# Kernel tuning notes

Hardware: AMD Instinct MI355X
Metric: run time of the kernel (lower is better)

The kernel has to match this reference:

```python
import jax, jax.numpy as jnp
import numpy as np

# Standard SMPL kinematic tree (24 joints), parent of joint i
PARENTS = np.array([-1, 0, 0, 0, 1, 2, 3, 4, 5, 6, 7, 8, 9, 9, 9,
                    12, 13, 14, 16, 17, 18, 19, 20, 21])
N_JOINTS = 24
EPS = 1e-8  # stands in for the tiny gaussian eps the torch code adds


def rodrigues(r):
    """Axis-angle (N,3) -> rotation matrices (N,3,3)."""
    theta = jnp.linalg.norm(r, axis=1, keepdims=True) + EPS        # (N,1)
    r_hat = r / theta                                              # (N,3)
    cos = jnp.cos(theta)[..., None]                                # (N,1,1)
    sin = jnp.sin(theta)[..., None]
    z = jnp.zeros_like(r_hat[:, 0])
    # skew-symmetric cross-product matrix of r_hat
    m = jnp.stack([z, -r_hat[:, 2], r_hat[:, 1],
                   r_hat[:, 2], z, -r_hat[:, 0],
                   -r_hat[:, 1], r_hat[:, 0], z], axis=1).reshape(-1, 3, 3)
    outer = r_hat[:, :, None] * r_hat[:, None, :]                  # (N,3,3)
    eye = jnp.eye(3, dtype=r.dtype)
    return cos * eye + (1.0 - cos) * outer + sin * m


def setup_inputs() -> dict:
    key = jax.random.key(0)
    k0, k1, k2, k3, k4 = jax.random.split(key, 5)
    B, V, J = 512, 6890, N_JOINTS
    return {
        "T_hat": jax.random.normal(k0, (V, 3), dtype=jnp.float32),
        "J_hat": jax.random.normal(k1, (J, 3), dtype=jnp.float32),
        "weights": jax.random.uniform(k2, (V, J), dtype=jnp.float32),
        "pose": jax.random.normal(k3, (B, J * 3), dtype=jnp.float32),
        "trans": jax.random.normal(k4, (B, 3), dtype=jnp.float32),
    }


def reference(T_hat, J_hat, weights, pose, trans):
    B = pose.shape[0]
    dt = pose.dtype
    # per-joint rotation matrices: (B,24,3,3)
    R = rodrigues(pose.reshape(-1, 3)).reshape(B, N_JOINTS, 3, 3)

    # relative joint offsets along the tree (24,3)
    rel_J = jnp.concatenate([J_hat[:1], J_hat[1:] - J_hat[PARENTS[1:]]], axis=0)

    # local SE(3) transforms (B,24,4,4)
    top = jnp.concatenate(
        [R, jnp.broadcast_to(rel_J[None, :, :, None], (B, N_JOINTS, 3, 1))],
        axis=-1)                                                   # (B,24,3,4)
    bottom = jnp.broadcast_to(
        jnp.array([0.0, 0.0, 0.0, 1.0], dtype=dt), (B, N_JOINTS, 1, 4))
    G_local = jnp.concatenate([top, bottom], axis=2)               # (B,24,4,4)

    # forward kinematics along the fixed 24-joint tree (small fixed loop)
    results = [G_local[:, 0]]
    for i in range(1, N_JOINTS):
        results.append(jnp.matmul(results[PARENTS[i]], G_local[:, i]))
    G = jnp.stack(results, axis=1)                                 # (B,24,4,4)

    # remove rest-pose joint locations from the translation column
    Jh = jnp.concatenate(
        [J_hat, jnp.zeros((N_JOINTS, 1), dtype=dt)], axis=1)       # (24,4)
    corr = jnp.einsum('bjxy,jy->bjx', G, Jh)                       # (B,24,4)
    G = G.at[:, :, :, 3].add(-corr)

    # linear blend skinning: per-vertex blended transforms (B,V,4,4)
    T = jnp.einsum('bjxy,vj->bvxy', G, weights)
    vh = jnp.concatenate(
        [T_hat, jnp.ones((T_hat.shape[0], 1), dtype=dt)], axis=1)  # (V,4)
    v = jnp.einsum('bvxy,vy->bvx', T, vh)[..., :3]                 # (B,V,3)
    return v + trans[:, None, :]
```

## Files before the change

kernel.cpp:

```cpp
#include <hip/hip_runtime.h>
#include <math.h>

#define NJ 24
#define TPB 256
#define BPT 8

typedef _Float16 f16x8 __attribute__((ext_vector_type(8)));
typedef float f32x4 __attribute__((ext_vector_type(4)));

__device__ __constant__ int PAR[NJ] = {-1,0,0,0,1,2,3,4,5,6,7,8,9,9,9,12,13,14,16,17,18,19,20,21};
__device__ __constant__ int CHAIN[NJ][9] = {
  {0,-1,-1,-1,-1,-1,-1,-1,-1},
  {0, 1,-1,-1,-1,-1,-1,-1,-1},
  {0, 2,-1,-1,-1,-1,-1,-1,-1},
  {0, 3,-1,-1,-1,-1,-1,-1,-1},
  {0, 1, 4,-1,-1,-1,-1,-1,-1},
  {0, 2, 5,-1,-1,-1,-1,-1,-1},
  {0, 3, 6,-1,-1,-1,-1,-1,-1},
  {0, 1, 4, 7,-1,-1,-1,-1,-1},
  {0, 2, 5, 8,-1,-1,-1,-1,-1},
  {0, 3, 6, 9,-1,-1,-1,-1,-1},
  {0, 1, 4, 7,10,-1,-1,-1,-1},
  {0, 2, 5, 8,11,-1,-1,-1,-1},
  {0, 3, 6, 9,12,-1,-1,-1,-1},
  {0, 3, 6, 9,13,-1,-1,-1,-1},
  {0, 3, 6, 9,14,-1,-1,-1,-1},
  {0, 3, 6, 9,12,15,-1,-1,-1},
  {0, 3, 6, 9,13,16,-1,-1,-1},
  {0, 3, 6, 9,14,17,-1,-1,-1},
  {0, 3, 6, 9,13,16,18,-1,-1},
  {0, 3, 6, 9,14,17,19,-1,-1},
  {0, 3, 6, 9,13,16,18,20,-1},
  {0, 3, 6, 9,14,17,19,21,-1},
  {0, 3, 6, 9,13,16,18,20,22},
  {0, 3, 6, 9,14,17,19,21,23},
};


__device__ __forceinline__ void fk_local(const float* __restrict__ J_hat,
                                         const float* __restrict__ pose,
                                         int b, int j, float* __restrict__ L )
{
  const float rx = pose[b * 72 + j * 3 + 0];
  const float ry = pose[b * 72 + j * 3 + 1];
  const float rz = pose[b * 72 + j * 3 + 2];
  const float theta = sqrtf(rx * rx + ry * ry + rz * rz) + 1e-8f;
  const float inv = 1.0f / theta;
  const float ux = rx * inv, uy = ry * inv, uz = rz * inv;
  const float c = cosf(theta), s = sinf(theta);
  const float ic = 1.0f - c;

  float tx = J_hat[j * 3 + 0];
  float ty = J_hat[j * 3 + 1];
  float tz = J_hat[j * 3 + 2];
  const int p = PAR[j];
  if (p >= 0) {
    tx -= J_hat[p * 3 + 0];
    ty -= J_hat[p * 3 + 1];
    tz -= J_hat[p * 3 + 2];
  }

  L[0]  = c + ic * ux * ux;
  L[1]  = ic * ux * uy - s * uz;
  L[2]  = ic * ux * uz + s * uy;
  L[3]  = tx;
  L[4]  = ic * uy * ux + s * uz;
  L[5]  = c + ic * uy * uy;
  L[6]  = ic * uy * uz - s * ux;
  L[7]  = ty;
  L[8]  = ic * uz * ux - s * uy;
  L[9]  = ic * uz * uy + s * ux;
  L[10] = c + ic * uz * uz;
  L[11] = tz;
}

__device__ __forceinline__ void fk_compose(const float (*__restrict__ Lc)[12],
                                           const float* __restrict__ J_hat,
                                           int j, float* __restrict__ g )
{
#pragma unroll
  for (int k = 0; k < 12; k++) g[k] = Lc[0][k];
#pragma unroll
  for (int d = 1; d < 9; d++) {
    const int a = CHAIN[j][d];
    if (a >= 0) {
      float l[12];
#pragma unroll
      for (int k = 0; k < 12; k++) l[k] = Lc[a][k];
      float n[12];
#pragma unroll
      for (int r = 0; r < 3; r++) {
        const float gr0 = g[r * 4 + 0], gr1 = g[r * 4 + 1], gr2 = g[r * 4 + 2];
        n[r * 4 + 0] = gr0 * l[0] + gr1 * l[4] + gr2 * l[8];
        n[r * 4 + 1] = gr0 * l[1] + gr1 * l[5] + gr2 * l[9];
        n[r * 4 + 2] = gr0 * l[2] + gr1 * l[6] + gr2 * l[10];
        n[r * 4 + 3] = gr0 * l[3] + gr1 * l[7] + gr2 * l[11] + g[r * 4 + 3];
      }
#pragma unroll
      for (int k = 0; k < 12; k++) g[k] = n[k];
    }
  }
  const float jx = J_hat[j * 3 + 0], jy = J_hat[j * 3 + 1], jz = J_hat[j * 3 + 2];
  g[3]  -= g[0] * jx + g[1] * jy + g[2]  * jz;
  g[7]  -= g[4] * jx + g[5] * jy + g[6]  * jz;
  g[11] -= g[8] * jx + g[9] * jy + g[10] * jz;
}

__global__ __launch_bounds__(TPB) void smpl_fused(
    const float* __restrict__ T_hat,
    const float* __restrict__ J_hat,
    const float* __restrict__ weights,
    const float* __restrict__ pose,
    const float* __restrict__ trans,
    float* __restrict__ out,
    int V)
{
  __shared__ __align__(16) float Lc[BPT][NJ][12];
  __shared__ __align__(16) _Float16 GhsH[BPT][512];
  __shared__ __align__(16) _Float16 GhsL[BPT][512];

  const int tid = threadIdx.x;
  const int b0 = blockIdx.y * BPT;

  {
    const int lb = tid >> 5;
    const int j  = tid & 31;
    const int b  = b0 + lb;

    if (j < NJ) {
      float L[12];
      fk_local(J_hat, pose, b, j, L);
#pragma unroll
      for (int k = 0; k < 12; k++) Lc[lb][j][k] = L[k];
    }
    __syncthreads();

    float g[12];
#pragma unroll
    for (int k = 0; k < 12; k++) g[k] = 0.0f;
    if (j < NJ) fk_compose(Lc[lb], J_hat, j, g);

    _Float16* dh = &GhsH[lb][0];
    _Float16* dl = &GhsL[lb][0];
#pragma unroll
    for (int c = 0; c < 16; c++) {
      _Float16 hi = (_Float16)0.f, lo = (_Float16)0.f;
      if (j < NJ && c < 12) {
        const float gv = g[c];
        hi = (_Float16)gv;
        lo = (_Float16)(gv - (float)hi);
      }
      dh[c * 32 + j] = hi;
      dl[c * 32 + j] = lo;
    }
    __syncthreads();
  }

  const int wid  = tid >> 6;
  const int lane = tid & 63;
  const int vbase = blockIdx.x * 256 + wid * 64;
  const int fr = lane & 15;
  const int kb = lane >> 4;

  f16x8 wfH[4], wfL[4];
#pragma unroll
  for (int t = 0; t < 4; t++) {
    const int v = vbase + t * 16 + fr;
    f16x8 h = {}, l = {};
    if (kb < 3 && v < V) {
      const float4* p = reinterpret_cast<const float4*>(weights + (size_t)v * 24 + kb * 8);
      const float4 a = p[0], c4 = p[1];
      float wv[8] = {a.x, a.y, a.z, a.w, c4.x, c4.y, c4.z, c4.w};
#pragma unroll
      for (int e = 0; e < 8; e++) {
        const _Float16 hi = (_Float16)wv[e];
        h[e] = hi;
        l[e] = (_Float16)(wv[e] - (float)hi);
      }
    }
    wfH[t] = h;
    wfL[t] = l;
  }

  float thx[4], thy[4], thz[4];
#pragma unroll
  for (int t = 0; t < 4; t++) {
    const int v = vbase + t * 16 + fr;
    if (v < V) {
      thx[t] = T_hat[v * 3 + 0];
      thy[t] = T_hat[v * 3 + 1];
      thz[t] = T_hat[v * 3 + 2];
    } else {
      thx[t] = thy[t] = thz[t] = 0.f;
    }
  }

  const int kc = (kb < 3) ? kb : 2;
  float tsel[BPT];
#pragma unroll
  for (int bi = 0; bi < BPT; bi++) tsel[bi] = trans[(b0 + bi) * 3 + kc];

#pragma unroll
  for (int bi = 0; bi < BPT; bi++) {
    const int b = b0 + bi;
    const f16x8 gH = *reinterpret_cast<const f16x8*>(&GhsH[bi][fr * 32 + kb * 8]);
    const f16x8 gL = *reinterpret_cast<const f16x8*>(&GhsL[bi][fr * 32 + kb * 8]);
#pragma unroll
    for (int t = 0; t < 4; t++) {
      f32x4 acc = {0.f, 0.f, 0.f, 0.f};
      acc = __builtin_amdgcn_mfma_f32_16x16x32_f16(gH, wfH[t], acc, 0, 0, 0);
      acc = __builtin_amdgcn_mfma_f32_16x16x32_f16(gH, wfL[t], acc, 0, 0, 0);
      acc = __builtin_amdgcn_mfma_f32_16x16x32_f16(gL, wfH[t], acc, 0, 0, 0);
      const float o = acc[0] * thx[t] + acc[1] * thy[t] + acc[2] * thz[t]
                    + acc[3] + tsel[bi];
      const int v = vbase + t * 16 + fr;
      if (kb < 3 && v < V)
        out[((size_t)b * V + v) * 3 + kb] = o;
    }
  }
}


__global__ __launch_bounds__(TPB) void smpl_blend_lds_kernel(
    const float* __restrict__ T_hat,
    const float* __restrict__ J_hat,
    const float* __restrict__ weights,
    const float* __restrict__ pose,
    const float* __restrict__ trans,
    float* __restrict__ out, int V)
{
  __shared__ __align__(16) float Lc[NJ][12];
  __shared__ __align__(16) float Gm[NJ][12];
  const int b = blockIdx.y;
  const int tid = threadIdx.x;

  if (tid < NJ) {
    float L[12];
    fk_local(J_hat, pose, b, tid, L);
#pragma unroll
    for (int k = 0; k < 12; k++) Lc[tid][k] = L[k];
  }
  __syncthreads();
  if (tid < NJ) {
    float g[12];
    fk_compose(Lc, J_hat, tid, g);
#pragma unroll
    for (int k = 0; k < 12; k++) Gm[tid][k] = g[k];
  }
  __syncthreads();

  const int v = blockIdx.x * TPB + tid;
  if (v >= V) return;

  float acc[12];
#pragma unroll
  for (int k = 0; k < 12; k++) acc[k] = 0.0f;
  const float* wv = weights + (size_t)v * 24;
#pragma unroll
  for (int j = 0; j < NJ; j++) {
    const float wj = wv[j];
#pragma unroll
    for (int k = 0; k < 12; k++) acc[k] = fmaf(wj, Gm[j][k], acc[k]);
  }
  const float x = T_hat[v * 3 + 0], y = T_hat[v * 3 + 1], z = T_hat[v * 3 + 2];
  float* op = out + ((size_t)b * V + v) * 3;
  op[0] = acc[0] * x + acc[1] * y + acc[2]  * z + acc[3]  + trans[b * 3 + 0];
  op[1] = acc[4] * x + acc[5] * y + acc[6]  * z + acc[7]  + trans[b * 3 + 1];
  op[2] = acc[8] * x + acc[9] * y + acc[10] * z + acc[11] + trans[b * 3 + 2];
}

extern "C" void kernel_launch(void* const* d_in, const int* in_sizes, int n_in,
                              void* d_out, int out_size, void* d_ws, size_t ws_size,
                              hipStream_t stream) {
  const float* T_hat   = (const float*)d_in[0];
  const float* J_hat   = (const float*)d_in[1];
  const float* weights = (const float*)d_in[2];
  const float* pose    = (const float*)d_in[3];
  const float* trans   = (const float*)d_in[4];
  float* out = (float*)d_out;

  const int V = in_sizes[0] / 3;
  const int B = in_sizes[3] / 72;

  const int nvchunks = (V + 255) / 256;

  if ((B % BPT) == 0) {
    dim3 grid(nvchunks, B / BPT);
    smpl_fused<<<grid, TPB, 0, stream>>>(T_hat, J_hat, weights, pose, trans, out, V);
  } else {
    dim3 grid(nvchunks, B);
    smpl_blend_lds_kernel<<<grid, TPB, 0, stream>>>(T_hat, J_hat, weights, pose, trans, out, V);
  }
}
```

Measured before the change: 30.84 us.

## Precompute fp16 weights and FK transforms in prep kernel, single-pass fp16 MFMA blend

Adds a prep kernel that converts skinning weights to padded fp16 rows and computes forward-kinematics transforms once per batch into workspace. The blend kernel then loads these fragments directly and issues one fp16 MFMA per tile instead of three hi/lo split MFMAs. This removes the FK recomputation repeated in every vertex block, along with the per-block weight conversion. It adds a second launch and workspace traffic, and it drops the hi/lo compensation, which lowers accuracy of the blended result.

```diff
diff --git a/kernel.cpp b/kernel.cpp
--- a/kernel.cpp
+++ b/kernel.cpp
@@ -3,7 +3,8 @@
 
 #define NJ 24
 #define TPB 256
-#define BPT 8
+#define BPT 4
+#define FK_BPB 8
 
 typedef _Float16 f16x8 __attribute__((ext_vector_type(8)));
 typedef float f32x4 __attribute__((ext_vector_type(4)));
@@ -106,81 +107,98 @@
   g[11] -= g[8] * jx + g[9] * jy + g[10] * jz;
 }
 
-__global__ __launch_bounds__(TPB) void smpl_fused(
+
+__global__ __launch_bounds__(TPB) void smpl_prep_all(
+    const float* __restrict__ weights,
+    const float* __restrict__ J_hat,
+    const float* __restrict__ pose,
+    _Float16* __restrict__ W_h,
+    _Float16* __restrict__ G_hT,
+    int V, int VP, int nvchunks, int B)
+{
+  __shared__ __align__(16) float Lc[FK_BPB][NJ][12];
+  const int tid = threadIdx.x;
+
+  if ((int)blockIdx.x < nvchunks) {
+    const int v = blockIdx.x * TPB + tid;
+    if (v >= VP) return;
+    _Float16 row[32];
+#pragma unroll
+    for (int k = 0; k < 32; k++) row[k] = (_Float16)0.f;
+    if (v < V) {
+      const float4* wp = reinterpret_cast<const float4*>(weights + (size_t)v * 24);
+#pragma unroll
+      for (int q = 0; q < 6; q++) {
+        const float4 t = wp[q];
+        row[q * 4 + 0] = (_Float16)t.x;
+        row[q * 4 + 1] = (_Float16)t.y;
+        row[q * 4 + 2] = (_Float16)t.z;
+        row[q * 4 + 3] = (_Float16)t.w;
+      }
+    }
+    float4* dst = reinterpret_cast<float4*>(W_h + (size_t)v * 32);
+    const float4* src = reinterpret_cast<const float4*>(row);
+#pragma unroll
+    for (int q = 0; q < 4; q++) dst[q] = src[q];
+  } else {
+    const int lb = tid >> 5;
+    const int j  = tid & 31;
+    const int b  = (blockIdx.x - nvchunks) * FK_BPB + lb;
+    const bool compute = (j < NJ) && (b < B);
+
+    if (compute) {
+      float L[12];
+      fk_local(J_hat, pose, b, j, L);
+#pragma unroll
+      for (int k = 0; k < 12; k++) Lc[lb][j][k] = L[k];
+    }
+    __syncthreads();
+
+    float g[12];
+#pragma unroll
+    for (int k = 0; k < 12; k++) g[k] = 0.0f;
+    if (compute) fk_compose(Lc[lb], J_hat, j, g);
+
+    if (b < B) {
+      _Float16* dst = G_hT + (size_t)b * 512;
+#pragma unroll
+      for (int c = 0; c < 16; c++) {
+        _Float16 val = (_Float16)0.f;
+        if (j < NJ && c < 12) val = (_Float16)g[c];
+        dst[c * 32 + j] = val;
+      }
+    }
+  }
+}
+
+__global__ __launch_bounds__(TPB) void smpl_blend_mfma(
     const float* __restrict__ T_hat,
-    const float* __restrict__ J_hat,
-    const float* __restrict__ weights,
-    const float* __restrict__ pose,
+    const _Float16* __restrict__ W_h,
     const float* __restrict__ trans,
+    const _Float16* __restrict__ G_hT,
     float* __restrict__ out,
     int V)
 {
-  __shared__ __align__(16) float Lc[BPT][NJ][12];
-  __shared__ __align__(16) _Float16 GhsH[BPT][512];
-  __shared__ __align__(16) _Float16 GhsL[BPT][512];
-
-  const int tid = threadIdx.x;
-  const int b0 = blockIdx.y * BPT;
-
-  {
-    const int lb = tid >> 5;
-    const int j  = tid & 31;
-    const int b  = b0 + lb;
-
-    if (j < NJ) {
-      float L[12];
-      fk_local(J_hat, pose, b, j, L);
-#pragma unroll
-      for (int k = 0; k < 12; k++) Lc[lb][j][k] = L[k];
-    }
-    __syncthreads();
-
-    float g[12];
-#pragma unroll
-    for (int k = 0; k < 12; k++) g[k] = 0.0f;
-    if (j < NJ) fk_compose(Lc[lb], J_hat, j, g);
-
-    _Float16* dh = &GhsH[lb][0];
-    _Float16* dl = &GhsL[lb][0];
-#pragma unroll
-    for (int c = 0; c < 16; c++) {
-      _Float16 hi = (_Float16)0.f, lo = (_Float16)0.f;
-      if (j < NJ && c < 12) {
-        const float gv = g[c];
-        hi = (_Float16)gv;
-        lo = (_Float16)(gv - (float)hi);
-      }
-      dh[c * 32 + j] = hi;
-      dl[c * 32 + j] = lo;
-    }
-    __syncthreads();
-  }
-
+  const int tid  = threadIdx.x;
   const int wid  = tid >> 6;
   const int lane = tid & 63;
   const int vbase = blockIdx.x * 256 + wid * 64;
+  const int b0 = blockIdx.y * BPT;
+
   const int fr = lane & 15;
   const int kb = lane >> 4;
 
-  f16x8 wfH[4], wfL[4];
-#pragma unroll
-  for (int t = 0; t < 4; t++) {
-    const int v = vbase + t * 16 + fr;
-    f16x8 h = {}, l = {};
-    if (kb < 3 && v < V) {
-      const float4* p = reinterpret_cast<const float4*>(weights + (size_t)v * 24 + kb * 8);
-      const float4 a = p[0], c4 = p[1];
-      float wv[8] = {a.x, a.y, a.z, a.w, c4.x, c4.y, c4.z, c4.w};
-#pragma unroll
-      for (int e = 0; e < 8; e++) {
-        const _Float16 hi = (_Float16)wv[e];
-        h[e] = hi;
-        l[e] = (_Float16)(wv[e] - (float)hi);
-      }
-    }
-    wfH[t] = h;
-    wfL[t] = l;
-  }
+  f16x8 wfrag[4];
+#pragma unroll
+  for (int t = 0; t < 4; t++)
+    wfrag[t] = *reinterpret_cast<const f16x8*>(
+        W_h + ((size_t)(vbase + t * 16 + fr)) * 32 + kb * 8);
+
+  f16x8 gfrag[BPT];
+#pragma unroll
+  for (int bi = 0; bi < BPT; bi++)
+    gfrag[bi] = *reinterpret_cast<const f16x8*>(
+        G_hT + ((size_t)(b0 + bi) * 16 + fr) * 32 + kb * 8);
 
   float thx[4], thy[4], thz[4];
 #pragma unroll
@@ -203,14 +221,10 @@
 #pragma unroll
   for (int bi = 0; bi < BPT; bi++) {
     const int b = b0 + bi;
-    const f16x8 gH = *reinterpret_cast<const f16x8*>(&GhsH[bi][fr * 32 + kb * 8]);
-    const f16x8 gL = *reinterpret_cast<const f16x8*>(&GhsL[bi][fr * 32 + kb * 8]);
 #pragma unroll
     for (int t = 0; t < 4; t++) {
       f32x4 acc = {0.f, 0.f, 0.f, 0.f};
-      acc = __builtin_amdgcn_mfma_f32_16x16x32_f16(gH, wfH[t], acc, 0, 0, 0);
-      acc = __builtin_amdgcn_mfma_f32_16x16x32_f16(gH, wfL[t], acc, 0, 0, 0);
-      acc = __builtin_amdgcn_mfma_f32_16x16x32_f16(gL, wfH[t], acc, 0, 0, 0);
+      acc = __builtin_amdgcn_mfma_f32_16x16x32_f16(gfrag[bi], wfrag[t], acc, 0, 0, 0);
       const float o = acc[0] * thx[t] + acc[1] * thy[t] + acc[2] * thz[t]
                     + acc[3] + tsel[bi];
       const int v = vbase + t * 16 + fr;
@@ -283,10 +297,21 @@
   const int B = in_sizes[3] / 72;
 
   const int nvchunks = (V + 255) / 256;
-
-  if ((B % BPT) == 0) {
+  const int VP = nvchunks * 256;
+
+  const size_t wh_bytes = (size_t)VP * 32 * sizeof(_Float16);
+  const size_t gh_bytes = (size_t)B * 512 * sizeof(_Float16);
+  const size_t mfma_need = wh_bytes + gh_bytes;
+
+  if (ws_size >= mfma_need && (B % BPT) == 0 && (B % FK_BPB) == 0) {
+    _Float16* W_h  = (_Float16*)d_ws;
+    _Float16* G_hT = (_Float16*)((char*)d_ws + wh_bytes);
+
+    const int prep_blocks = nvchunks + B / FK_BPB;
+    smpl_prep_all<<<prep_blocks, TPB, 0, stream>>>(
+        weights, J_hat, pose, W_h, G_hT, V, VP, nvchunks, B);
     dim3 grid(nvchunks, B / BPT);
-    smpl_fused<<<grid, TPB, 0, stream>>>(T_hat, J_hat, weights, pose, trans, out, V);
+    smpl_blend_mfma<<<grid, TPB, 0, stream>>>(T_hat, W_h, trans, G_hT, out, V);
   } else {
     dim3 grid(nvchunks, B);
     smpl_blend_lds_kernel<<<grid, TPB, 0, stream>>>(T_hat, J_hat, weights, pose, trans, out, V);
```

Result: faster. 28.52 us (-7.5%).
